# Optimization experiments

Measured on AMD Instinct MI355X. Metric: run time of the kernel, lower is better.

## Reference

```python
import jax, jax.numpy as jnp
import numpy as np

jax.config.update("jax_enable_x64", True)

NUM_PARTS = 4
N_CAD = 8192
N_CAM = 8192


def setup_inputs() -> dict:
    key = jax.random.key(0)
    ks = jax.random.split(key, 7)
    cad_pts = jax.random.normal(ks[0], (NUM_PARTS, N_CAD, 3), jnp.float32)
    camera_pts = jax.random.normal(ks[1], (NUM_PARTS, N_CAM, 3), jnp.float32)
    part_weight = jax.random.uniform(ks[2], (NUM_PARTS,), jnp.float32)
    rot_quats = jax.random.normal(ks[3], (NUM_PARTS, 4), jnp.float32)  # [w,x,y,z] per part
    tras = 0.1 * jax.random.normal(ks[4], (NUM_PARTS, 3, 1), jnp.float32)
    rt_k = jnp.eye(4, dtype=jnp.float32)[None] + 0.01 * jax.random.normal(ks[5], (NUM_PARTS, 4, 4), jnp.float32)
    joint_axes = jax.random.normal(ks[6], (NUM_PARTS - 1, 2, 4), jnp.float32)
    return {"camera_pts": camera_pts, "cad_pts": cad_pts, "part_weight": part_weight,
            "rot_quats": rot_quats, "tras": tras, "rt_k": rt_k, "joint_axes": joint_axes}


def _quat_to_rot(q):
    # q = [w, x, y, z] -> a,b,c,d as in the torch code
    q = q / jnp.linalg.norm(q)
    a, b, c, d = q[0], q[1], q[2], q[3]
    return jnp.stack([
        1 - 2 * c * c - 2 * d * d, 2 * b * c - 2 * a * d, 2 * a * c + 2 * b * d,
        2 * b * c + 2 * a * d, 1 - 2 * b * b - 2 * d * d, 2 * c * d - 2 * a * b,
        2 * b * d - 2 * a * c, 2 * a * b + 2 * c * d, 1 - 2 * b * b - 2 * c * c,
    ]).reshape(3, 3)


def _chamfer(x, y):
    # symmetric Chamfer (mean of k=1 NN distances both ways), in float64 like torch code
    x = x.astype(jnp.float64)
    y = y.astype(jnp.float64)
    x2 = jnp.sum(x * x, axis=1)  # [N]
    y2 = jnp.sum(y * y, axis=1)  # [M]
    d2 = x2[:, None] + y2[None, :] - 2.0 * (x @ y.T)  # [N,M]
    d = jnp.sqrt(jnp.maximum(d2, 0.0))
    return jnp.min(d, axis=1).mean() + jnp.min(d, axis=0).mean()


def _forward(camera_pts, cad_pts, part_weight, rot_quats, tras, rt_k, joint_axes):
    P = cad_pts.shape[0]
    f32 = jnp.float32
    # homogeneous coords [P,N,4] / [P,M,4]
    scad = jnp.concatenate([cad_pts, jnp.ones(cad_pts.shape[:2] + (1,), f32)], axis=-1)
    scam = jnp.concatenate([camera_pts, jnp.ones(camera_pts.shape[:2] + (1,), f32)], axis=-1)

    rots = jax.vmap(_quat_to_rot)(rot_quats)                       # [P,3,3]
    top = jnp.concatenate([rots, tras], axis=2)                    # [P,3,4]
    bottom = jnp.broadcast_to(jnp.array([[[0.0, 0.0, 0.0, 1.0]]], f32), (P, 1, 4))
    transforms = jnp.concatenate([top, bottom], axis=1)            # [P,4,4]

    cad_base = jnp.einsum('pij,pnj->pni', transforms, scad)        # [P,N,4]
    e_geo = jax.vmap(_chamfer)(cad_base, scam)                     # [P] float64
    eners = 5.0 * e_geo                                            # [P]

    # torch.tensor(eners) detaches -> stop_gradient
    et = jax.lax.stop_gradient(eners)
    et = (et - jnp.min(et)) / (jnp.max(et) - jnp.min(et) + 1e-8)
    sm = jax.nn.softmax(et, axis=0)                                # [P] float64

    errors_p = part_weight.astype(jnp.float64) * sm * eners        # [P]
    all_obj = jnp.sum(sm * eners)

    # ---- E_kin ----
    x_t = jnp.einsum('pij,pnj->pni', transforms, scad)             # [P,N,4]
    distances = jnp.linalg.norm(x_t - scam, axis=-1).mean(axis=-1).mean()
    Tj_q = rt_k[0] @ transforms[0] @ joint_axes[0, 0]              # [4] (fixed index 0, as in source)
    Tj1_q = jnp.einsum('pij,pjk,pk->pi', rt_k[1:], transforms[1:], joint_axes[:, 1])  # [P-1,4]
    diff = (Tj_q[None, :] - Tj1_q)[:, :3]                          # [P-1,3]
    nrm = jnp.linalg.norm(diff) / P
    e_kin = jnp.log(0.1 * nrm + 1.0) + distances

    e_kin_total = jnp.max(errors_p) * e_kin
    all_obj = all_obj + e_kin_total
    errors = jnp.concatenate([errors_p, e_kin_total[None]])        # [P+1]
    return all_obj, errors, jax.lax.stop_gradient(transforms)


def reference(camera_pts, cad_pts, part_weight, rot_quats, tras, rt_k, joint_axes):
    return _forward(camera_pts, cad_pts, part_weight, rot_quats, tras, rt_k, joint_axes)
```

## Files before the change

kernel.cpp:

```cpp
#include <hip/hip_runtime.h>
#include <cstdint>
#include <math.h>

#define NPARTS 4
#define NPTS   8192

#define WS_SUMS_OFF 256
#define WS_MIN_OFF  384

__global__ __launch_bounds__(256) void k_setup(const float* __restrict__ rot_quats,
                                               const float* __restrict__ tras,
                                               float* __restrict__ ws,
                                               float* __restrict__ out) {
    uint32_t* minbuf = (uint32_t*)((char*)ws + WS_MIN_OFF);
    int gid = blockIdx.x * blockDim.x + threadIdx.x;
    int nthr = gridDim.x * blockDim.x;
    for (int i = gid; i < 2 * NPARTS * NPTS; i += nthr) minbuf[i] = 0x7F800000u;
    if (blockIdx.x == 0) {
        if (threadIdx.x >= 16 && threadIdx.x < 25) {
            double* s = (double*)((char*)ws + WS_SUMS_OFF);
            s[threadIdx.x - 16] = 0.0;
        }
        if (threadIdx.x < NPARTS) {
            int p = threadIdx.x;
            double q0 = rot_quats[p*4+0], q1 = rot_quats[p*4+1];
            double q2 = rot_quats[p*4+2], q3 = rot_quats[p*4+3];
            double inv = 1.0 / sqrt(q0*q0 + q1*q1 + q2*q2 + q3*q3);
            double a = q0*inv, b = q1*inv, c = q2*inv, d = q3*inv;
            float T[16];
            T[0]  = (float)(1.0 - 2.0*c*c - 2.0*d*d);
            T[1]  = (float)(2.0*b*c - 2.0*a*d);
            T[2]  = (float)(2.0*a*c + 2.0*b*d);
            T[3]  = tras[p*3+0];
            T[4]  = (float)(2.0*b*c + 2.0*a*d);
            T[5]  = (float)(1.0 - 2.0*b*b - 2.0*d*d);
            T[6]  = (float)(2.0*c*d - 2.0*a*b);
            T[7]  = tras[p*3+1];
            T[8]  = (float)(2.0*b*d - 2.0*a*c);
            T[9]  = (float)(2.0*a*b + 2.0*c*d);
            T[10] = (float)(1.0 - 2.0*b*b - 2.0*c*c);
            T[11] = tras[p*3+2];
            T[12] = 0.f; T[13] = 0.f; T[14] = 0.f; T[15] = 1.f;
            #pragma unroll
            for (int i = 0; i < 16; ++i) {
                ws[p*16 + i] = T[i];
                out[6 + p*16 + i] = T[i];
            }
        }
    }
}

__global__ __launch_bounds__(256, 2) void k_chamfer(const float* __restrict__ cam,
                                                    const float* __restrict__ cad,
                                                    float* __restrict__ ws) {
    constexpr int TPB = 256, REG_X = 8;
    constexpr int XTILE = TPB * REG_X;
    constexpr int XTILES = NPTS / XTILE;
    constexpr int YSPLIT = 16;
    constexpr int YLEN = NPTS / YSPLIT;
    __shared__ float4 ybuf[YLEN];

    uint32_t* minbuf = (uint32_t*)((char*)ws + WS_MIN_OFF);

    int b   = blockIdx.x;
    int ysi = b & (YSPLIT - 1);
    int xt  = (b / YSPLIT) & (XTILES - 1);
    int dir = (b / (YSPLIT * XTILES)) & 1;
    int p   = b / (YSPLIT * XTILES * 2);

    float T[12];
    #pragma unroll
    for (int i = 0; i < 12; ++i) T[i] = ws[p*16 + i];

    const float* xsrc = (dir == 0) ? cad + (size_t)p*NPTS*3 : cam + (size_t)p*NPTS*3;
    const float* ysrc = (dir == 0) ? cam + (size_t)p*NPTS*3 : cad + (size_t)p*NPTS*3;

    for (int j = threadIdx.x; j < YLEN; j += TPB) {
        int yi = ysi * YLEN + j;
        float v0 = ysrc[yi*3+0], v1 = ysrc[yi*3+1], v2 = ysrc[yi*3+2];
        if (dir == 1) {
            float w0 = T[0]*v0 + T[1]*v1 + T[2]*v2 + T[3];
            float w1 = T[4]*v0 + T[5]*v1 + T[6]*v2 + T[7];
            float w2 = T[8]*v0 + T[9]*v1 + T[10]*v2 + T[11];
            v0 = w0; v1 = w1; v2 = w2;
        }
        ybuf[j] = make_float4(-2.f*v0, -2.f*v1, -2.f*v2, v0*v0 + v1*v1 + v2*v2);
    }

    float x0[REG_X], x1[REG_X], x2c[REG_X], xsq[REG_X];
    #pragma unroll
    for (int r = 0; r < REG_X; ++r) {
        int xi = xt*XTILE + r*TPB + threadIdx.x;
        float v0 = xsrc[xi*3+0], v1 = xsrc[xi*3+1], v2 = xsrc[xi*3+2];
        if (dir == 0) {
            float w0 = T[0]*v0 + T[1]*v1 + T[2]*v2 + T[3];
            float w1 = T[4]*v0 + T[5]*v1 + T[6]*v2 + T[7];
            float w2 = T[8]*v0 + T[9]*v1 + T[10]*v2 + T[11];
            v0 = w0; v1 = w1; v2 = w2;
        }
        x0[r] = v0; x1[r] = v1; x2c[r] = v2;
        xsq[r] = v0*v0 + v1*v1 + v2*v2;
    }

    float mnA[REG_X], mnB[REG_X];
    #pragma unroll
    for (int r = 0; r < REG_X; ++r) { mnA[r] = INFINITY; mnB[r] = INFINITY; }

    __syncthreads();

    #pragma unroll 2
    for (int j = 0; j < YLEN; j += 2) {
        float4 ya = ybuf[j];
        float4 yb = ybuf[j+1];
        #pragma unroll
        for (int r = 0; r < REG_X; ++r) {
            float ta = fmaf(x0[r], ya.x, ya.w);
            ta = fmaf(x1[r], ya.y, ta);
            ta = fmaf(x2c[r], ya.z, ta);
            mnA[r] = fminf(mnA[r], ta);
            float tb = fmaf(x0[r], yb.x, yb.w);
            tb = fmaf(x1[r], yb.y, tb);
            tb = fmaf(x2c[r], yb.z, tb);
            mnB[r] = fminf(mnB[r], tb);
        }
    }

    #pragma unroll
    for (int r = 0; r < REG_X; ++r) {
        int xi = xt*XTILE + r*TPB + threadIdx.x;
        float d2 = fmaxf(xsq[r] + fminf(mnA[r], mnB[r]), 0.f);
        atomicMin(&minbuf[(dir*NPARTS + p)*NPTS + xi], __float_as_uint(d2));
    }
}

__global__ __launch_bounds__(256) void k_dist(const float* __restrict__ cam,
                                              const float* __restrict__ cad,
                                              float* __restrict__ ws) {
    int gid = blockIdx.x * 256 + threadIdx.x;
    int p = gid >> 13;
    float T[12];
    #pragma unroll
    for (int i = 0; i < 12; ++i) T[i] = ws[p*16 + i];
    float v0 = cad[gid*3+0], v1 = cad[gid*3+1], v2 = cad[gid*3+2];
    float w0 = T[0]*v0 + T[1]*v1 + T[2]*v2 + T[3];
    float w1 = T[4]*v0 + T[5]*v1 + T[6]*v2 + T[7];
    float w2 = T[8]*v0 + T[9]*v1 + T[10]*v2 + T[11];
    float d0 = w0 - cam[gid*3+0];
    float d1 = w1 - cam[gid*3+1];
    float d2 = w2 - cam[gid*3+2];
    double local = sqrt((double)(d0*d0 + d1*d1 + d2*d2));

    __shared__ double red[256];
    red[threadIdx.x] = local;
    __syncthreads();
    for (int s = 128; s > 0; s >>= 1) {
        if (threadIdx.x < s) red[threadIdx.x] += red[threadIdx.x + s];
        __syncthreads();
    }
    if (threadIdx.x == 0) {
        double* dist_sum = (double*)((char*)ws + WS_SUMS_OFF) + 8;
        atomicAdd(dist_sum, red[0]);
    }
}

__global__ __launch_bounds__(256) void k_reduce(float* __restrict__ ws) {
    uint32_t* minbuf = (uint32_t*)((char*)ws + WS_MIN_OFF);
    double* sums = (double*)((char*)ws + WS_SUMS_OFF);
    int b = blockIdx.x;
    int dir = b >> 5;
    int p = (b >> 3) & 3;
    int base = b * 1024;
    double local = 0.0;
    #pragma unroll
    for (int k = 0; k < 4; ++k) {
        uint32_t bits = minbuf[base + k*256 + threadIdx.x];
        local += sqrt((double)__uint_as_float(bits));
    }
    __shared__ double red[256];
    red[threadIdx.x] = local;
    __syncthreads();
    for (int s = 128; s > 0; s >>= 1) {
        if (threadIdx.x < s) red[threadIdx.x] += red[threadIdx.x + s];
        __syncthreads();
    }
    if (threadIdx.x == 0) atomicAdd(&sums[p*2 + dir], red[0]);
}

__global__ void k_final(const float* __restrict__ pw,
                        const float* __restrict__ rtk,
                        const float* __restrict__ ja,
                        const float* __restrict__ ws,
                        float* __restrict__ out) {
    const double* sums = (const double*)((const char*)ws + WS_SUMS_OFF);
    double eners[NPARTS];
    for (int p = 0; p < NPARTS; ++p)
        eners[p] = 5.0 * ((sums[p*2+0] + sums[p*2+1]) / (double)NPTS);

    double mn = eners[0], mx = eners[0];
    for (int p = 1; p < NPARTS; ++p) { mn = fmin(mn, eners[p]); mx = fmax(mx, eners[p]); }
    double et[NPARTS], etmax = -1e300;
    for (int p = 0; p < NPARTS; ++p) { et[p] = (eners[p] - mn) / (mx - mn + 1e-8); etmax = fmax(etmax, et[p]); }
    double ex[NPARTS], se = 0.0;
    for (int p = 0; p < NPARTS; ++p) { ex[p] = exp(et[p] - etmax); se += ex[p]; }

    double ep[NPARTS], all_obj = 0.0, epmax = -1e300;
    for (int p = 0; p < NPARTS; ++p) {
        double sm = ex[p] / se;
        ep[p] = (double)pw[p] * sm * eners[p];
        all_obj += sm * eners[p];
        epmax = fmax(epmax, ep[p]);
    }

    double distances = sums[8] / (double)(NPARTS * NPTS);

    double v[4], Tj[4], ss = 0.0;
    for (int i = 0; i < 4; ++i) {
        v[i] = 0.0;
        for (int k = 0; k < 4; ++k) v[i] += (double)ws[0*16 + i*4 + k] * (double)ja[0*8 + 0*4 + k];
    }
    for (int i = 0; i < 4; ++i) {
        Tj[i] = 0.0;
        for (int k = 0; k < 4; ++k) Tj[i] += (double)rtk[0*16 + i*4 + k] * v[k];
    }
    for (int q = 1; q < NPARTS; ++q) {
        double vv[4], u[4];
        for (int i = 0; i < 4; ++i) {
            vv[i] = 0.0;
            for (int k = 0; k < 4; ++k) vv[i] += (double)ws[q*16 + i*4 + k] * (double)ja[(q-1)*8 + 4 + k];
        }
        for (int i = 0; i < 4; ++i) {
            u[i] = 0.0;
            for (int k = 0; k < 4; ++k) u[i] += (double)rtk[q*16 + i*4 + k] * vv[k];
        }
        for (int i = 0; i < 3; ++i) { double dd = Tj[i] - u[i]; ss += dd * dd; }
    }
    double nrm = sqrt(ss) / (double)NPARTS;
    double e_kin = log(0.1 * nrm + 1.0) + distances;
    double ekt = epmax * e_kin;
    all_obj += ekt;

    out[0] = (float)all_obj;
    for (int p = 0; p < NPARTS; ++p) out[1 + p] = (float)ep[p];
    out[5] = (float)ekt;
}

extern "C" void kernel_launch(void* const* d_in, const int* in_sizes, int n_in,
                              void* d_out, int out_size, void* d_ws, size_t ws_size,
                              hipStream_t stream) {
    const float* cam  = (const float*)d_in[0];
    const float* cad  = (const float*)d_in[1];
    const float* pw   = (const float*)d_in[2];
    const float* rq   = (const float*)d_in[3];
    const float* tras = (const float*)d_in[4];
    const float* rtk  = (const float*)d_in[5];
    const float* ja   = (const float*)d_in[6];
    float* out = (float*)d_out;
    float* ws  = (float*)d_ws;

    hipLaunchKernelGGL(k_setup,   dim3(64),  dim3(256), 0, stream, rq, tras, ws, out);
    hipLaunchKernelGGL(k_chamfer, dim3(512), dim3(256), 0, stream, cam, cad, ws);
    hipLaunchKernelGGL(k_dist,    dim3(128), dim3(256), 0, stream, cam, cad, ws);
    hipLaunchKernelGGL(k_reduce,  dim3(64),  dim3(256), 0, stream, ws);
    hipLaunchKernelGGL(k_final,   dim3(1),   dim3(1),   0, stream, pw, rtk, ja, ws, out);
}
```

Measured before the change: 57.01 us.

## Use packed FMA and min3 in chamfer, double Y split, merge dist into reduce

The chamfer inner loop now uses v_pk_fma_f32 to evaluate two candidate points per instruction and v_min3_f32 to fold both into the running min. The y tile is stored as separate per-component arrays. YSPLIT is doubled to 32, giving 1024 blocks, and launch bounds move to 4 blocks per CU. The k_dist kernel is folded into k_reduce to save one launch. Together these aim to cut VALU instruction count in the hot loop and improve occupancy, at the cost of twice as many atomicMin writes and twice as many y-tile loads.

```diff
diff --git a/kernel.cpp b/kernel.cpp
--- a/kernel.cpp
+++ b/kernel.cpp
@@ -7,6 +7,20 @@
 
 #define WS_SUMS_OFF 256
 #define WS_MIN_OFF  384
+
+typedef float f32x2 __attribute__((ext_vector_type(2)));
+typedef float f32x4 __attribute__((ext_vector_type(4)));
+
+__device__ __forceinline__ f32x2 pk_fma(f32x2 a, f32x2 b, f32x2 c) {
+    f32x2 d;
+    asm("v_pk_fma_f32 %0, %1, %2, %3" : "=v"(d) : "v"(a), "v"(b), "v"(c));
+    return d;
+}
+__device__ __forceinline__ float min3f(float a, float b, float c) {
+    float d;
+    asm("v_min3_f32 %0, %1, %2, %3" : "=v"(d) : "v"(a), "v"(b), "v"(c));
+    return d;
+}
 
 __global__ __launch_bounds__(256) void k_setup(const float* __restrict__ rot_quats,
                                                const float* __restrict__ tras,
@@ -50,15 +64,15 @@
     }
 }
 
-__global__ __launch_bounds__(256, 2) void k_chamfer(const float* __restrict__ cam,
+__global__ __launch_bounds__(256, 4) void k_chamfer(const float* __restrict__ cam,
                                                     const float* __restrict__ cad,
                                                     float* __restrict__ ws) {
     constexpr int TPB = 256, REG_X = 8;
     constexpr int XTILE = TPB * REG_X;
     constexpr int XTILES = NPTS / XTILE;
-    constexpr int YSPLIT = 16;
+    constexpr int YSPLIT = 32;
     constexpr int YLEN = NPTS / YSPLIT;
-    __shared__ float4 ybuf[YLEN];
+    __shared__ f32x4 ybuf4[4][YLEN / 4];
 
     uint32_t* minbuf = (uint32_t*)((char*)ws + WS_MIN_OFF);
 
@@ -75,7 +89,8 @@
     const float* xsrc = (dir == 0) ? cad + (size_t)p*NPTS*3 : cam + (size_t)p*NPTS*3;
     const float* ysrc = (dir == 0) ? cam + (size_t)p*NPTS*3 : cad + (size_t)p*NPTS*3;
 
-    for (int j = threadIdx.x; j < YLEN; j += TPB) {
+    {
+        int j = threadIdx.x;
         int yi = ysi * YLEN + j;
         float v0 = ysrc[yi*3+0], v1 = ysrc[yi*3+1], v2 = ysrc[yi*3+2];
         if (dir == 1) {
@@ -84,10 +99,13 @@
             float w2 = T[8]*v0 + T[9]*v1 + T[10]*v2 + T[11];
             v0 = w0; v1 = w1; v2 = w2;
         }
-        ybuf[j] = make_float4(-2.f*v0, -2.f*v1, -2.f*v2, v0*v0 + v1*v1 + v2*v2);
-    }
-
-    float x0[REG_X], x1[REG_X], x2c[REG_X], xsq[REG_X];
+        ((float*)ybuf4[0])[j] = -2.f * v0;
+        ((float*)ybuf4[1])[j] = -2.f * v1;
+        ((float*)ybuf4[2])[j] = -2.f * v2;
+        ((float*)ybuf4[3])[j] = v0*v0 + v1*v1 + v2*v2;
+    }
+
+    f32x2 x0pk[REG_X], x1pk[REG_X], x2pk[REG_X];
     #pragma unroll
     for (int r = 0; r < REG_X; ++r) {
         int xi = xt*XTILE + r*TPB + threadIdx.x;
@@ -98,92 +116,99 @@
             float w2 = T[8]*v0 + T[9]*v1 + T[10]*v2 + T[11];
             v0 = w0; v1 = w1; v2 = w2;
         }
-        x0[r] = v0; x1[r] = v1; x2c[r] = v2;
-        xsq[r] = v0*v0 + v1*v1 + v2*v2;
-    }
-
-    float mnA[REG_X], mnB[REG_X];
-    #pragma unroll
-    for (int r = 0; r < REG_X; ++r) { mnA[r] = INFINITY; mnB[r] = INFINITY; }
+        x0pk[r] = (f32x2){v0, v0};
+        x1pk[r] = (f32x2){v1, v1};
+        x2pk[r] = (f32x2){v2, v2};
+    }
+
+    float mn[REG_X];
+    #pragma unroll
+    for (int r = 0; r < REG_X; ++r) mn[r] = INFINITY;
 
     __syncthreads();
 
-    #pragma unroll 2
-    for (int j = 0; j < YLEN; j += 2) {
-        float4 ya = ybuf[j];
-        float4 yb = ybuf[j+1];
+    for (int g = 0; g < YLEN / 4; ++g) {
+        f32x4 c0 = ybuf4[0][g];
+        f32x4 c1 = ybuf4[1][g];
+        f32x4 c2 = ybuf4[2][g];
+        f32x4 qq = ybuf4[3][g];
+        f32x2 c0lo = __builtin_shufflevector(c0, c0, 0, 1), c0hi = __builtin_shufflevector(c0, c0, 2, 3);
+        f32x2 c1lo = __builtin_shufflevector(c1, c1, 0, 1), c1hi = __builtin_shufflevector(c1, c1, 2, 3);
+        f32x2 c2lo = __builtin_shufflevector(c2, c2, 0, 1), c2hi = __builtin_shufflevector(c2, c2, 2, 3);
+        f32x2 qqlo = __builtin_shufflevector(qq, qq, 0, 1), qqhi = __builtin_shufflevector(qq, qq, 2, 3);
         #pragma unroll
         for (int r = 0; r < REG_X; ++r) {
-            float ta = fmaf(x0[r], ya.x, ya.w);
-            ta = fmaf(x1[r], ya.y, ta);
-            ta = fmaf(x2c[r], ya.z, ta);
-            mnA[r] = fminf(mnA[r], ta);
-            float tb = fmaf(x0[r], yb.x, yb.w);
-            tb = fmaf(x1[r], yb.y, tb);
-            tb = fmaf(x2c[r], yb.z, tb);
-            mnB[r] = fminf(mnB[r], tb);
+            f32x2 t = pk_fma(x0pk[r], c0lo, qqlo);
+            t = pk_fma(x1pk[r], c1lo, t);
+            t = pk_fma(x2pk[r], c2lo, t);
+            mn[r] = min3f(mn[r], t.x, t.y);
+            f32x2 u = pk_fma(x0pk[r], c0hi, qqhi);
+            u = pk_fma(x1pk[r], c1hi, u);
+            u = pk_fma(x2pk[r], c2hi, u);
+            mn[r] = min3f(mn[r], u.x, u.y);
         }
     }
 
     #pragma unroll
     for (int r = 0; r < REG_X; ++r) {
         int xi = xt*XTILE + r*TPB + threadIdx.x;
-        float d2 = fmaxf(xsq[r] + fminf(mnA[r], mnB[r]), 0.f);
+        float v0 = x0pk[r].x, v1 = x1pk[r].x, v2 = x2pk[r].x;
+        float d2 = fmaxf(v0*v0 + v1*v1 + v2*v2 + mn[r], 0.f);
         atomicMin(&minbuf[(dir*NPARTS + p)*NPTS + xi], __float_as_uint(d2));
     }
 }
 
-__global__ __launch_bounds__(256) void k_dist(const float* __restrict__ cam,
-                                              const float* __restrict__ cad,
-                                              float* __restrict__ ws) {
-    int gid = blockIdx.x * 256 + threadIdx.x;
-    int p = gid >> 13;
-    float T[12];
-    #pragma unroll
-    for (int i = 0; i < 12; ++i) T[i] = ws[p*16 + i];
-    float v0 = cad[gid*3+0], v1 = cad[gid*3+1], v2 = cad[gid*3+2];
-    float w0 = T[0]*v0 + T[1]*v1 + T[2]*v2 + T[3];
-    float w1 = T[4]*v0 + T[5]*v1 + T[6]*v2 + T[7];
-    float w2 = T[8]*v0 + T[9]*v1 + T[10]*v2 + T[11];
-    float d0 = w0 - cam[gid*3+0];
-    float d1 = w1 - cam[gid*3+1];
-    float d2 = w2 - cam[gid*3+2];
-    double local = sqrt((double)(d0*d0 + d1*d1 + d2*d2));
-
+__global__ __launch_bounds__(256) void k_reduce(const float* __restrict__ cam,
+                                                const float* __restrict__ cad,
+                                                float* __restrict__ ws) {
     __shared__ double red[256];
-    red[threadIdx.x] = local;
-    __syncthreads();
-    for (int s = 128; s > 0; s >>= 1) {
-        if (threadIdx.x < s) red[threadIdx.x] += red[threadIdx.x + s];
+    double local = 0.0;
+    int b = blockIdx.x;
+    if (b < 64) {
+        uint32_t* minbuf = (uint32_t*)((char*)ws + WS_MIN_OFF);
+        int base = b * 1024;
+        #pragma unroll
+        for (int k = 0; k < 4; ++k) {
+            uint32_t bits = minbuf[base + k*256 + threadIdx.x];
+            local += sqrt((double)__uint_as_float(bits));
+        }
+        red[threadIdx.x] = local;
         __syncthreads();
-    }
-    if (threadIdx.x == 0) {
-        double* dist_sum = (double*)((char*)ws + WS_SUMS_OFF) + 8;
-        atomicAdd(dist_sum, red[0]);
-    }
-}
-
-__global__ __launch_bounds__(256) void k_reduce(float* __restrict__ ws) {
-    uint32_t* minbuf = (uint32_t*)((char*)ws + WS_MIN_OFF);
-    double* sums = (double*)((char*)ws + WS_SUMS_OFF);
-    int b = blockIdx.x;
-    int dir = b >> 5;
-    int p = (b >> 3) & 3;
-    int base = b * 1024;
-    double local = 0.0;
-    #pragma unroll
-    for (int k = 0; k < 4; ++k) {
-        uint32_t bits = minbuf[base + k*256 + threadIdx.x];
-        local += sqrt((double)__uint_as_float(bits));
-    }
-    __shared__ double red[256];
-    red[threadIdx.x] = local;
-    __syncthreads();
-    for (int s = 128; s > 0; s >>= 1) {
-        if (threadIdx.x < s) red[threadIdx.x] += red[threadIdx.x + s];
+        for (int s = 128; s > 0; s >>= 1) {
+            if (threadIdx.x < s) red[threadIdx.x] += red[threadIdx.x + s];
+            __syncthreads();
+        }
+        if (threadIdx.x == 0) {
+            double* sums = (double*)((char*)ws + WS_SUMS_OFF);
+            int dir = b >> 5;
+            int p = (b >> 3) & 3;
+            atomicAdd(&sums[p*2 + dir], red[0]);
+        }
+    } else {
+        int gid = (b - 64) * 256 + threadIdx.x;
+        int p = gid >> 13;
+        float T[12];
+        #pragma unroll
+        for (int i = 0; i < 12; ++i) T[i] = ws[p*16 + i];
+        float v0 = cad[gid*3+0], v1 = cad[gid*3+1], v2 = cad[gid*3+2];
+        float w0 = T[0]*v0 + T[1]*v1 + T[2]*v2 + T[3];
+        float w1 = T[4]*v0 + T[5]*v1 + T[6]*v2 + T[7];
+        float w2 = T[8]*v0 + T[9]*v1 + T[10]*v2 + T[11];
+        float d0 = w0 - cam[gid*3+0];
+        float d1 = w1 - cam[gid*3+1];
+        float d2 = w2 - cam[gid*3+2];
+        local = sqrt((double)(d0*d0 + d1*d1 + d2*d2));
+        red[threadIdx.x] = local;
         __syncthreads();
-    }
-    if (threadIdx.x == 0) atomicAdd(&sums[p*2 + dir], red[0]);
+        for (int s = 128; s > 0; s >>= 1) {
+            if (threadIdx.x < s) red[threadIdx.x] += red[threadIdx.x + s];
+            __syncthreads();
+        }
+        if (threadIdx.x == 0) {
+            double* dist_sum = (double*)((char*)ws + WS_SUMS_OFF) + 8;
+            atomicAdd(dist_sum, red[0]);
+        }
+    }
 }
 
 __global__ void k_final(const float* __restrict__ pw,
@@ -257,9 +282,8 @@
     float* out = (float*)d_out;
     float* ws  = (float*)d_ws;
 
-    hipLaunchKernelGGL(k_setup,   dim3(64),  dim3(256), 0, stream, rq, tras, ws, out);
-    hipLaunchKernelGGL(k_chamfer, dim3(512), dim3(256), 0, stream, cam, cad, ws);
-    hipLaunchKernelGGL(k_dist,    dim3(128), dim3(256), 0, stream, cam, cad, ws);
-    hipLaunchKernelGGL(k_reduce,  dim3(64),  dim3(256), 0, stream, ws);
-    hipLaunchKernelGGL(k_final,   dim3(1),   dim3(1),   0, stream, pw, rtk, ja, ws, out);
-}
+    hipLaunchKernelGGL(k_setup,   dim3(64),   dim3(256), 0, stream, rq, tras, ws, out);
+    hipLaunchKernelGGL(k_chamfer, dim3(1024), dim3(256), 0, stream, cam, cad, ws);
+    hipLaunchKernelGGL(k_reduce,  dim3(192),  dim3(256), 0, stream, cam, cad, ws);
+    hipLaunchKernelGGL(k_final,   dim3(1),    dim3(1),   0, stream, pw, rtk, ja, ws, out);
+}
```

Result: faster. 55.42 us (-2.8%).

## Compute chamfer distances with bf16 split MFMA and argmin index packing

Applied to the files above, without the earlier changes.

Replaces the scalar FMA nearest-neighbour loop with 32x32x16 bf16 MFMA, using a hi/lo bf16 split of coordinates and squared norms so the matrix product approximates the squared distance. The neighbour index is packed into the low mantissa bits so a min also yields an argmin. The exact distance is then recomputed in double from the stored points during reduction. Per-ysplit partial minima replace global atomicMin, and the transform and distance-sum kernels are fused into one preprocessing kernel. The cost is extra workspace traffic, and the bf16 approximation risks choosing a wrong neighbour when candidates are nearly tied.

```diff
diff --git a/kernel.cpp b/kernel.cpp
--- a/kernel.cpp
+++ b/kernel.cpp
@@ -4,186 +4,245 @@
 
 #define NPARTS 4
 #define NPTS   8192
-
-#define WS_SUMS_OFF 256
-#define WS_MIN_OFF  384
-
-__global__ __launch_bounds__(256) void k_setup(const float* __restrict__ rot_quats,
-                                               const float* __restrict__ tras,
-                                               float* __restrict__ ws,
-                                               float* __restrict__ out) {
-    uint32_t* minbuf = (uint32_t*)((char*)ws + WS_MIN_OFF);
-    int gid = blockIdx.x * blockDim.x + threadIdx.x;
-    int nthr = gridDim.x * blockDim.x;
-    for (int i = gid; i < 2 * NPARTS * NPTS; i += nthr) minbuf[i] = 0x7F800000u;
-    if (blockIdx.x == 0) {
-        if (threadIdx.x >= 16 && threadIdx.x < 25) {
-            double* s = (double*)((char*)ws + WS_SUMS_OFF);
-            s[threadIdx.x - 16] = 0.0;
-        }
-        if (threadIdx.x < NPARTS) {
-            int p = threadIdx.x;
-            double q0 = rot_quats[p*4+0], q1 = rot_quats[p*4+1];
-            double q2 = rot_quats[p*4+2], q3 = rot_quats[p*4+3];
-            double inv = 1.0 / sqrt(q0*q0 + q1*q1 + q2*q2 + q3*q3);
-            double a = q0*inv, b = q1*inv, c = q2*inv, d = q3*inv;
-            float T[16];
-            T[0]  = (float)(1.0 - 2.0*c*c - 2.0*d*d);
-            T[1]  = (float)(2.0*b*c - 2.0*a*d);
-            T[2]  = (float)(2.0*a*c + 2.0*b*d);
-            T[3]  = tras[p*3+0];
-            T[4]  = (float)(2.0*b*c + 2.0*a*d);
-            T[5]  = (float)(1.0 - 2.0*b*b - 2.0*d*d);
-            T[6]  = (float)(2.0*c*d - 2.0*a*b);
-            T[7]  = tras[p*3+1];
-            T[8]  = (float)(2.0*b*d - 2.0*a*c);
-            T[9]  = (float)(2.0*a*b + 2.0*c*d);
-            T[10] = (float)(1.0 - 2.0*b*b - 2.0*c*c);
-            T[11] = tras[p*3+2];
-            T[12] = 0.f; T[13] = 0.f; T[14] = 0.f; T[15] = 1.f;
-            #pragma unroll
-            for (int i = 0; i < 16; ++i) {
-                ws[p*16 + i] = T[i];
-                out[6 + p*16 + i] = T[i];
-            }
-        }
-    }
-}
-
-__global__ __launch_bounds__(256, 2) void k_chamfer(const float* __restrict__ cam,
-                                                    const float* __restrict__ cad,
-                                                    float* __restrict__ ws) {
-    constexpr int TPB = 256, REG_X = 8;
-    constexpr int XTILE = TPB * REG_X;
-    constexpr int XTILES = NPTS / XTILE;
-    constexpr int YSPLIT = 16;
-    constexpr int YLEN = NPTS / YSPLIT;
-    __shared__ float4 ybuf[YLEN];
-
-    uint32_t* minbuf = (uint32_t*)((char*)ws + WS_MIN_OFF);
-
-    int b   = blockIdx.x;
-    int ysi = b & (YSPLIT - 1);
-    int xt  = (b / YSPLIT) & (XTILES - 1);
-    int dir = (b / (YSPLIT * XTILES)) & 1;
-    int p   = b / (YSPLIT * XTILES * 2);
+#define YSPLIT 8
+#define XT     64
+
+#define WS_SUMS_OFF 0
+#define WS_T_OFF    128
+#define KVB_OFF     1024
+#define PTS_OFF     (KVB_OFF + 2097152)
+#define PART_OFF    (PTS_OFF + 1048576)
+
+typedef __bf16 bf16x8 __attribute__((ext_vector_type(8)));
+typedef float  f32x4  __attribute__((ext_vector_type(4)));
+typedef float  f32x16 __attribute__((ext_vector_type(16)));
+
+__device__ __forceinline__ float min3f(float a, float b, float c) {
+    float d;
+    asm("v_min3_f32 %0, %1, %2, %3" : "=v"(d) : "v"(a), "v"(b), "v"(c));
+    return d;
+}
+
+__device__ __forceinline__ void make_T(const float* __restrict__ rq,
+                                       const float* __restrict__ tras,
+                                       int p, float* T) {
+    float q0 = rq[p*4+0], q1 = rq[p*4+1], q2 = rq[p*4+2], q3 = rq[p*4+3];
+    float inv = 1.0f / sqrtf(q0*q0 + q1*q1 + q2*q2 + q3*q3);
+    float a = q0*inv, b = q1*inv, c = q2*inv, d = q3*inv;
+    T[0]  = 1.f - 2.f*c*c - 2.f*d*d;
+    T[1]  = 2.f*b*c - 2.f*a*d;
+    T[2]  = 2.f*a*c + 2.f*b*d;
+    T[3]  = tras[p*3+0];
+    T[4]  = 2.f*b*c + 2.f*a*d;
+    T[5]  = 1.f - 2.f*b*b - 2.f*d*d;
+    T[6]  = 2.f*c*d - 2.f*a*b;
+    T[7]  = tras[p*3+1];
+    T[8]  = 2.f*b*d - 2.f*a*c;
+    T[9]  = 2.f*a*b + 2.f*c*d;
+    T[10] = 1.f - 2.f*b*b - 2.f*c*c;
+    T[11] = tras[p*3+2];
+}
+
+__global__ __launch_bounds__(256) void k_pre(const float* __restrict__ cam,
+                                             const float* __restrict__ cad,
+                                             const float* __restrict__ rq,
+                                             const float* __restrict__ tras,
+                                             float* __restrict__ ws,
+                                             float* __restrict__ out) {
+    int gid = blockIdx.x * 256 + threadIdx.x;
+    int set = gid >> 15;
+    int p   = (gid >> 13) & 3;
+    int i   = gid & (NPTS - 1);
 
     float T[12];
+    make_T(rq, tras, p, T);
+
+    float w0, w1, w2;
+    float c0 = 0.f, c1 = 0.f, c2 = 0.f;
+    if (set == 0) {
+        float v0 = cad[(size_t)(p*NPTS + i)*3 + 0];
+        float v1 = cad[(size_t)(p*NPTS + i)*3 + 1];
+        float v2 = cad[(size_t)(p*NPTS + i)*3 + 2];
+        w0 = fmaf(T[0], v0, fmaf(T[1], v1, fmaf(T[2],  v2, T[3])));
+        w1 = fmaf(T[4], v0, fmaf(T[5], v1, fmaf(T[6],  v2, T[7])));
+        w2 = fmaf(T[8], v0, fmaf(T[9], v1, fmaf(T[10], v2, T[11])));
+        c0 = cam[(size_t)(p*NPTS + i)*3 + 0];
+        c1 = cam[(size_t)(p*NPTS + i)*3 + 1];
+        c2 = cam[(size_t)(p*NPTS + i)*3 + 2];
+    } else {
+        w0 = cam[(size_t)(p*NPTS + i)*3 + 0];
+        w1 = cam[(size_t)(p*NPTS + i)*3 + 1];
+        w2 = cam[(size_t)(p*NPTS + i)*3 + 2];
+    }
+
+    float Xs = w0*w0 + w1*w1 + w2*w2;
+
+    f32x4* pts = (f32x4*)((char*)ws + PTS_OFF);
+    size_t sp = (size_t)(set*4 + p);
+    pts[sp*NPTS + i] = (f32x4){w0, w1, w2, Xs};
+
+    __bf16 h0 = (__bf16)w0, h1 = (__bf16)w1, h2 = (__bf16)w2;
+    __bf16 l0 = (__bf16)(w0 - (float)h0);
+    __bf16 l1 = (__bf16)(w1 - (float)h1);
+    __bf16 l2 = (__bf16)(w2 - (float)h2);
+    __bf16 sh = (__bf16)Xs;
+    __bf16 sl = (__bf16)(Xs - (float)sh);
+    __bf16 one = (__bf16)1.0f;
+
+    bf16x8 B0 = {h0, h1, h2, l0, l1, l2, h0, h1};
+    bf16x8 B1 = {h2, l0, l1, l2, one, one, sh, sl};
+
+    uint4* kvb = (uint4*)((char*)ws + KVB_OFF);
+    kvb[(sp*2 + 0)*NPTS + i] = __builtin_bit_cast(uint4, B0);
+    kvb[(sp*2 + 1)*NPTS + i] = __builtin_bit_cast(uint4, B1);
+
+    if (blockIdx.x == 0 && threadIdx.x < 4) {
+        float Tt[12];
+        make_T(rq, tras, threadIdx.x, Tt);
+        float* wsT = ws + WS_T_OFF/4 + threadIdx.x*16;
+        float* outT = out + 6 + threadIdx.x*16;
+        #pragma unroll
+        for (int k = 0; k < 12; ++k) { wsT[k] = Tt[k]; outT[k] = Tt[k]; }
+        wsT[12] = 0.f; wsT[13] = 0.f; wsT[14] = 0.f; wsT[15] = 1.f;
+        outT[12] = 0.f; outT[13] = 0.f; outT[14] = 0.f; outT[15] = 1.f;
+    }
+
+    if (set == 0) {
+        float d0 = w0 - c0, d1 = w1 - c1, d2 = w2 - c2;
+        double local = sqrt((double)(d0*d0 + d1*d1 + d2*d2));
+        __shared__ double red[256];
+        red[threadIdx.x] = local;
+        __syncthreads();
+        for (int s = 128; s > 0; s >>= 1) {
+            if (threadIdx.x < s) red[threadIdx.x] += red[threadIdx.x + s];
+            __syncthreads();
+        }
+        if (threadIdx.x == 0)
+            atomicAdd((double*)((char*)ws + WS_SUMS_OFF) + 8, red[0]);
+    }
+}
+
+__global__ __launch_bounds__(256, 2) void k_chamfer(float* __restrict__ ws) {
+    const int tid  = threadIdx.x;
+    const int lane = tid & 63;
+    const int wv   = tid >> 6;
+    const int col  = lane & 31;
+    const int half = lane >> 5;
+
+    const int b   = blockIdx.x;
+    const int ys  = b & (YSPLIT - 1);
+    const int xt  = (b >> 3) & (XT - 1);
+    const int p   = (b >> 9) & 3;
+    const int dir = b >> 11;
+    const int setA = dir;
+    const int setB = 1 - dir;
+
+    __shared__ uint4 ywin[2048];
+
+    const uint4* kvb = (const uint4*)((const char*)ws + KVB_OFF) + ((size_t)(setB*4 + p)*2)*NPTS;
+    const f32x4* ptsA = (const f32x4*)((const char*)ws + PTS_OFF) + (size_t)(setA*4 + p)*NPTS;
+    const int ywin0 = ys * 1024;
+
+    for (int i = tid; i < 2048; i += 256) {
+        int h = i >> 10, c = i & 1023;
+        ywin[i] = kvb[(size_t)h*NPTS + ywin0 + c];
+    }
+
+    const int rowbase = xt*128 + wv*32;
+    bf16x8 af;
+    {
+        f32x4 X = ptsA[rowbase + col];
+        float w0 = X.x, w1 = X.y, w2 = X.z, Xs = X.w;
+        __bf16 h0 = (__bf16)w0, h1 = (__bf16)w1, h2 = (__bf16)w2;
+        __bf16 l0 = (__bf16)(w0 - (float)h0);
+        __bf16 l1 = (__bf16)(w1 - (float)h1);
+        __bf16 l2 = (__bf16)(w2 - (float)h2);
+        __bf16 sh = (__bf16)Xs;
+        __bf16 sl = (__bf16)(Xs - (float)sh);
+        __bf16 one = (__bf16)1.0f;
+        __bf16 m0 = (__bf16)(-2.f*(float)h0), m1 = (__bf16)(-2.f*(float)h1), m2 = (__bf16)(-2.f*(float)h2);
+        __bf16 n0 = (__bf16)(-2.f*(float)l0), n1 = (__bf16)(-2.f*(float)l1), n2 = (__bf16)(-2.f*(float)l2);
+        bf16x8 A0 = {m0, m1, m2, m0, m1, m2, n0, n1};
+        bf16x8 A1 = {n2, n0, n1, n2, sh, sl, one, one};
+        af = half ? A1 : A0;
+    }
+
+    f32x16 Z = {0,0,0,0,0,0,0,0,0,0,0,0,0,0,0,0};
+    float rm[16];
     #pragma unroll
-    for (int i = 0; i < 12; ++i) T[i] = ws[p*16 + i];
-
-    const float* xsrc = (dir == 0) ? cad + (size_t)p*NPTS*3 : cam + (size_t)p*NPTS*3;
-    const float* ysrc = (dir == 0) ? cam + (size_t)p*NPTS*3 : cad + (size_t)p*NPTS*3;
-
-    for (int j = threadIdx.x; j < YLEN; j += TPB) {
-        int yi = ysi * YLEN + j;
-        float v0 = ysrc[yi*3+0], v1 = ysrc[yi*3+1], v2 = ysrc[yi*3+2];
-        if (dir == 1) {
-            float w0 = T[0]*v0 + T[1]*v1 + T[2]*v2 + T[3];
-            float w1 = T[4]*v0 + T[5]*v1 + T[6]*v2 + T[7];
-            float w2 = T[8]*v0 + T[9]*v1 + T[10]*v2 + T[11];
-            v0 = w0; v1 = w1; v2 = w2;
-        }
-        ybuf[j] = make_float4(-2.f*v0, -2.f*v1, -2.f*v2, v0*v0 + v1*v1 + v2*v2);
-    }
-
-    float x0[REG_X], x1[REG_X], x2c[REG_X], xsq[REG_X];
+    for (int i = 0; i < 16; ++i) rm[i] = INFINITY;
+
+    __syncthreads();
+
+    const int hbase = half * 1024;
+    const uint32_t ipack0 = (uint32_t)(ywin0 + col);
+    #pragma unroll 4
+    for (int s = 0; s < 32; s += 2) {
+        bf16x8 b0 = __builtin_bit_cast(bf16x8, ywin[hbase + (s+0)*32 + col]);
+        bf16x8 b1 = __builtin_bit_cast(bf16x8, ywin[hbase + (s+1)*32 + col]);
+        f32x16 a0 = __builtin_amdgcn_mfma_f32_32x32x16_bf16(af, b0, Z, 0, 0, 0);
+        f32x16 a1 = __builtin_amdgcn_mfma_f32_32x32x16_bf16(af, b1, Z, 0, 0, 0);
+        const uint32_t i0 = ipack0 + (uint32_t)(s*32);
+        const uint32_t i1 = i0 + 32u;
+        #pragma unroll
+        for (int i = 0; i < 16; ++i) {
+            uint32_t u0 = (__float_as_uint(a0[i]) & 0xFFFFE000u) | i0;
+            uint32_t u1 = (__float_as_uint(a1[i]) & 0xFFFFE000u) | i1;
+            rm[i] = min3f(rm[i], __uint_as_float(u0), __uint_as_float(u1));
+        }
+    }
+
     #pragma unroll
-    for (int r = 0; r < REG_X; ++r) {
-        int xi = xt*XTILE + r*TPB + threadIdx.x;
-        float v0 = xsrc[xi*3+0], v1 = xsrc[xi*3+1], v2 = xsrc[xi*3+2];
-        if (dir == 0) {
-            float w0 = T[0]*v0 + T[1]*v1 + T[2]*v2 + T[3];
-            float w1 = T[4]*v0 + T[5]*v1 + T[6]*v2 + T[7];
-            float w2 = T[8]*v0 + T[9]*v1 + T[10]*v2 + T[11];
-            v0 = w0; v1 = w1; v2 = w2;
-        }
-        x0[r] = v0; x1[r] = v1; x2c[r] = v2;
-        xsq[r] = v0*v0 + v1*v1 + v2*v2;
-    }
-
-    float mnA[REG_X], mnB[REG_X];
-    #pragma unroll
-    for (int r = 0; r < REG_X; ++r) { mnA[r] = INFINITY; mnB[r] = INFINITY; }
-
-    __syncthreads();
-
-    #pragma unroll 2
-    for (int j = 0; j < YLEN; j += 2) {
-        float4 ya = ybuf[j];
-        float4 yb = ybuf[j+1];
-        #pragma unroll
-        for (int r = 0; r < REG_X; ++r) {
-            float ta = fmaf(x0[r], ya.x, ya.w);
-            ta = fmaf(x1[r], ya.y, ta);
-            ta = fmaf(x2c[r], ya.z, ta);
-            mnA[r] = fminf(mnA[r], ta);
-            float tb = fmaf(x0[r], yb.x, yb.w);
-            tb = fmaf(x1[r], yb.y, tb);
-            tb = fmaf(x2c[r], yb.z, tb);
-            mnB[r] = fminf(mnB[r], tb);
-        }
-    }
-
-    #pragma unroll
-    for (int r = 0; r < REG_X; ++r) {
-        int xi = xt*XTILE + r*TPB + threadIdx.x;
-        float d2 = fmaxf(xsq[r] + fminf(mnA[r], mnB[r]), 0.f);
-        atomicMin(&minbuf[(dir*NPARTS + p)*NPTS + xi], __float_as_uint(d2));
-    }
-}
-
-__global__ __launch_bounds__(256) void k_dist(const float* __restrict__ cam,
-                                              const float* __restrict__ cad,
-                                              float* __restrict__ ws) {
-    int gid = blockIdx.x * 256 + threadIdx.x;
-    int p = gid >> 13;
-    float T[12];
-    #pragma unroll
-    for (int i = 0; i < 12; ++i) T[i] = ws[p*16 + i];
-    float v0 = cad[gid*3+0], v1 = cad[gid*3+1], v2 = cad[gid*3+2];
-    float w0 = T[0]*v0 + T[1]*v1 + T[2]*v2 + T[3];
-    float w1 = T[4]*v0 + T[5]*v1 + T[6]*v2 + T[7];
-    float w2 = T[8]*v0 + T[9]*v1 + T[10]*v2 + T[11];
-    float d0 = w0 - cam[gid*3+0];
-    float d1 = w1 - cam[gid*3+1];
-    float d2 = w2 - cam[gid*3+2];
-    double local = sqrt((double)(d0*d0 + d1*d1 + d2*d2));
-
+    for (int m = 1; m <= 16; m <<= 1) {
+        #pragma unroll
+        for (int i = 0; i < 16; ++i)
+            rm[i] = fminf(rm[i], __shfl_xor(rm[i], m, 64));
+    }
+
+    if (col == 0) {
+        float* rowpart = (float*)((char*)ws + PART_OFF) + ((size_t)((dir*4 + p)*YSPLIT + ys))*NPTS + rowbase;
+        #pragma unroll
+        for (int i = 0; i < 16; ++i) {
+            int row = (i & 3) + 8*(i >> 2) + 4*half;
+            rowpart[row] = rm[i];
+        }
+    }
+}
+
+__global__ __launch_bounds__(256) void k_reduce(float* __restrict__ ws) {
     __shared__ double red[256];
-    red[threadIdx.x] = local;
-    __syncthreads();
-    for (int s = 128; s > 0; s >>= 1) {
-        if (threadIdx.x < s) red[threadIdx.x] += red[threadIdx.x + s];
-        __syncthreads();
-    }
-    if (threadIdx.x == 0) {
-        double* dist_sum = (double*)((char*)ws + WS_SUMS_OFF) + 8;
-        atomicAdd(dist_sum, red[0]);
-    }
-}
-
-__global__ __launch_bounds__(256) void k_reduce(float* __restrict__ ws) {
-    uint32_t* minbuf = (uint32_t*)((char*)ws + WS_MIN_OFF);
-    double* sums = (double*)((char*)ws + WS_SUMS_OFF);
-    int b = blockIdx.x;
-    int dir = b >> 5;
-    int p = (b >> 3) & 3;
-    int base = b * 1024;
+    const int b = blockIdx.x;
+    const int tid = threadIdx.x;
+    const int dir = b >> 5, p = (b >> 3) & 3, seg = b & 7;
+    const int setA = dir, setB = 1 - dir;
+    const float* part = (const float*)((const char*)ws + PART_OFF) + ((size_t)(dir*4 + p))*YSPLIT*NPTS;
+    const f32x4* pts  = (const f32x4*)((const char*)ws + PTS_OFF);
+    const f32x4* xp = pts + (size_t)(setA*4 + p)*NPTS;
+    const f32x4* ypt = pts + (size_t)(setB*4 + p)*NPTS;
     double local = 0.0;
     #pragma unroll
     for (int k = 0; k < 4; ++k) {
-        uint32_t bits = minbuf[base + k*256 + threadIdx.x];
-        local += sqrt((double)__uint_as_float(bits));
-    }
-    __shared__ double red[256];
-    red[threadIdx.x] = local;
+        int row = seg*1024 + k*256 + tid;
+        float m = INFINITY;
+        #pragma unroll
+        for (int y = 0; y < YSPLIT; ++y)
+            m = fminf(m, part[(size_t)y*NPTS + row]);
+        uint32_t idx = __float_as_uint(m) & 0x1FFFu;
+        f32x4 X = xp[row];
+        f32x4 Y = ypt[idx];
+        double d0 = (double)X.x - (double)Y.x;
+        double d1 = (double)X.y - (double)Y.y;
+        double d2 = (double)X.z - (double)Y.z;
+        local += sqrt(fmax(d0*d0 + d1*d1 + d2*d2, 0.0));
+    }
+    red[tid] = local;
     __syncthreads();
     for (int s = 128; s > 0; s >>= 1) {
-        if (threadIdx.x < s) red[threadIdx.x] += red[threadIdx.x + s];
+        if (tid < s) red[tid] += red[tid + s];
         __syncthreads();
     }
-    if (threadIdx.x == 0) atomicAdd(&sums[p*2 + dir], red[0]);
+    if (tid == 0)
+        atomicAdd((double*)((char*)ws + WS_SUMS_OFF) + p*2 + dir, red[0]);
 }
 
 __global__ void k_final(const float* __restrict__ pw,
@@ -192,6 +251,7 @@
                         const float* __restrict__ ws,
                         float* __restrict__ out) {
     const double* sums = (const double*)((const char*)ws + WS_SUMS_OFF);
+    const float* Tw = ws + WS_T_OFF/4;
     double eners[NPARTS];
     for (int p = 0; p < NPARTS; ++p)
         eners[p] = 5.0 * ((sums[p*2+0] + sums[p*2+1]) / (double)NPTS);
@@ -216,7 +276,7 @@
     double v[4], Tj[4], ss = 0.0;
     for (int i = 0; i < 4; ++i) {
         v[i] = 0.0;
-        for (int k = 0; k < 4; ++k) v[i] += (double)ws[0*16 + i*4 + k] * (double)ja[0*8 + 0*4 + k];
+        for (int k = 0; k < 4; ++k) v[i] += (double)Tw[0*16 + i*4 + k] * (double)ja[0*8 + 0*4 + k];
     }
     for (int i = 0; i < 4; ++i) {
         Tj[i] = 0.0;
@@ -226,7 +286,7 @@
         double vv[4], u[4];
         for (int i = 0; i < 4; ++i) {
             vv[i] = 0.0;
-            for (int k = 0; k < 4; ++k) vv[i] += (double)ws[q*16 + i*4 + k] * (double)ja[(q-1)*8 + 4 + k];
+            for (int k = 0; k < 4; ++k) vv[i] += (double)Tw[q*16 + i*4 + k] * (double)ja[(q-1)*8 + 4 + k];
         }
         for (int i = 0; i < 4; ++i) {
             u[i] = 0.0;
@@ -257,9 +317,9 @@
     float* out = (float*)d_out;
     float* ws  = (float*)d_ws;
 
-    hipLaunchKernelGGL(k_setup,   dim3(64),  dim3(256), 0, stream, rq, tras, ws, out);
-    hipLaunchKernelGGL(k_chamfer, dim3(512), dim3(256), 0, stream, cam, cad, ws);
-    hipLaunchKernelGGL(k_dist,    dim3(128), dim3(256), 0, stream, cam, cad, ws);
-    hipLaunchKernelGGL(k_reduce,  dim3(64),  dim3(256), 0, stream, ws);
-    hipLaunchKernelGGL(k_final,   dim3(1),   dim3(1),   0, stream, pw, rtk, ja, ws, out);
-}
+    hipMemsetAsync(ws, 0, 128, stream);
+    hipLaunchKernelGGL(k_pre,     dim3(256),  dim3(256), 0, stream, cam, cad, rq, tras, ws, out);
+    hipLaunchKernelGGL(k_chamfer, dim3(4096), dim3(256), 0, stream, ws);
+    hipLaunchKernelGGL(k_reduce,  dim3(64),   dim3(256), 0, stream, ws);
+    hipLaunchKernelGGL(k_final,   dim3(1),    dim3(1),   0, stream, pw, rtk, ja, ws, out);
+}
```

Measured after the change: 69.58 us. 1.22x slower.
